# Optimization experiments

Hardware: AMD Instinct MI355X
Metric: run time of the kernel (lower is better)

Reference implementation:

```python
import jax, jax.numpy as jnp
import numpy as np

B, S, D, H = 2, 2048, 512, 8
DK = D // H

def setup_inputs() -> dict:
    key = jax.random.key(0)
    ks = jax.random.split(key, 13)
    inp = {
        'query': jax.random.normal(ks[0], (B, S, D), jnp.float32),
        'key': jax.random.normal(ks[1], (B, S, D), jnp.float32),
        'value': jax.random.normal(ks[2], (B, S, D), jnp.float32),
        'group_prob': jax.random.uniform(ks[3], (B, S, S), jnp.float32),
        'mask': jax.random.randint(ks[4], (B, S, S), 0, 2, jnp.int32),
        'Wq': jax.random.normal(ks[5], (D, D), jnp.float32) * 0.02,
        'bq': jax.random.normal(ks[6], (D,), jnp.float32) * 0.02,
        'Wk': jax.random.normal(ks[7], (D, D), jnp.float32) * 0.02,
        'bk': jax.random.normal(ks[8], (D,), jnp.float32) * 0.02,
        'Wv': jax.random.normal(ks[9], (D, D), jnp.float32) * 0.02,
        'bv': jax.random.normal(ks[10], (D,), jnp.float32) * 0.02,
        'Wo': jax.random.normal(ks[11], (D, D), jnp.float32) * 0.02,
        'bo': jax.random.normal(ks[12], (D,), jnp.float32) * 0.02,
    }
    return inp

def reference(query, key, value, group_prob, mask, Wq, bq, Wk, bk, Wv, bv, Wo, bo):
    # project and split heads: [B,S,D] -> [B,H,S,dk]
    def proj(x, W, b):
        return (x @ W.T + b).reshape(B, S, H, DK).transpose(0, 2, 1, 3)
    q = proj(query, Wq, bq)
    k = proj(key, Wk, bk)
    v = proj(value, Wv, bv)
    scale = 1.0 / np.sqrt(DK).astype(np.float32)
    scores = jnp.einsum('bhqd,bhkd->bhqk', q, k) * scale  # [B,H,S,S]
    # allowed = mask | identity-diagonal; disallowed positions get -1e9
    diag = jnp.eye(S, dtype=bool)
    allowed = (mask.astype(bool) | diag)[:, None, :, :]  # [B,1,S,S]
    scores = jnp.where(allowed, scores, jnp.float32(-1e9))
    p_attn = jax.nn.softmax(scores, axis=-1) * group_prob[:, None, :, :]
    # dropout is identity in eval/deterministic mode
    x = jnp.einsum('bhqk,bhkd->bhqd', p_attn, v)  # [B,H,S,dk]
    x = x.transpose(0, 2, 1, 3).reshape(B, S, D)
    return x @ Wo.T + bo
```

## Files before the change

### kernel.cpp

```cpp
#include <hip/hip_runtime.h>
#include <hip/hip_bf16.h>
#include <cstdint>
#include <cstddef>

typedef __attribute__((ext_vector_type(8))) short bf16x8;
typedef __attribute__((ext_vector_type(4))) float f32x4;
typedef __attribute__((address_space(3))) void lds_void;
typedef const __attribute__((address_space(1))) void g_void;

constexpr int Bc = 2, Sc = 2048, Dc = 512, Hc = 8, DKc = 64;
constexpr int SPLIT = 2;
constexpr int NKT = Sc / 64;
constexpr int KT_PER = NKT / SPLIT;
constexpr float CSC = 0.18033688011112042f;

struct alignas(16) us8 { unsigned short u[8]; };
struct alignas(8) us4 { unsigned short u[4]; };

__device__ __forceinline__ unsigned short f2bf(float x) {
  union { float f; unsigned int u; } v; v.f = x;
  unsigned int r = (v.u + 0x7FFFu + ((v.u >> 16) & 1u)) >> 16;
  return (unsigned short)r;
}

__device__ __forceinline__ us8 cvt8(float4 a, float4 b) {
  us8 o;
  o.u[0] = f2bf(a.x); o.u[1] = f2bf(a.y); o.u[2] = f2bf(a.z); o.u[3] = f2bf(a.w);
  o.u[4] = f2bf(b.x); o.u[5] = f2bf(b.y); o.u[6] = f2bf(b.z); o.u[7] = f2bf(b.w);
  return o;
}

struct CArgs { const float* src[7]; unsigned short* dst[7]; int n8[7]; };

__global__ __launch_bounds__(256)
void cvt_multi(CArgs a)
{
  const int y = blockIdx.y;
  const float* s = a.src[y];
  unsigned short* d = a.dst[y];
  const int n8 = a.n8[y];
  int i = blockIdx.x * blockDim.x + threadIdx.x;
  const int stride = gridDim.x * blockDim.x;
  for (; i < n8; i += stride) {
    float4 va = ((const float4*)s)[(size_t)i * 2];
    float4 vb = ((const float4*)s)[(size_t)i * 2 + 1];
    ((us8*)d)[i] = cvt8(va, vb);
  }
}

__global__ __launch_bounds__(256)
void cvt_mask(const int* __restrict__ m, unsigned long long* __restrict__ out, int ngroups)
{
  const int lane = threadIdx.x & 63;
  int gid = (blockIdx.x * blockDim.x + threadIdx.x) >> 6;
  const int stride = (gridDim.x * blockDim.x) >> 6;
  for (; gid < ngroups; gid += stride) {
    const size_t base = (size_t)gid * 64;
    const int rem = (int)(base & ((size_t)Sc * Sc - 1));
    const int srow = rem >> 11;
    const int k = (rem & (Sc - 1)) + lane;
    const bool pred = (m[base + lane] != 0) || (k == srow);
    unsigned long long bal = __ballot(pred);
    if (lane == 0) out[gid] = bal;
  }
}

struct GArgs {
  const unsigned short* A[3];
  const unsigned short* W[3];
  const float* bias[3];
  void* C[3];
  int mode[3];
};

__global__ __launch_bounds__(256)
void gemm128(GArgs ga)
{
  __shared__ unsigned short As[128][64];
  __shared__ unsigned short Bs[128][64];

  constexpr int K = 512, N = 512;
  const int z = blockIdx.z;
  const unsigned short* Ap = ga.A[z];
  const unsigned short* Wp = ga.W[z];
  const float* bias = ga.bias[z];
  const int mode = ga.mode[z];

  const int tid = threadIdx.x, lane = tid & 63, w = tid >> 6;
  const int m0 = blockIdx.x * 128, n0 = blockIdx.y * 128;
  const int wm = w >> 1, wn = w & 1;
  const int colb = lane & 15, hi = lane >> 4, rowb = hi * 4;
  const int swz = (colb & 7) << 4;

  f32x4 acc[4][4];
#pragma unroll
  for (int i = 0; i < 4; ++i)
#pragma unroll
    for (int j = 0; j < 4; ++j) acc[i][j] = (f32x4){0.f, 0.f, 0.f, 0.f};

  const int lrow8 = lane >> 3;
  const int cb = ((lane & 7) * 16) ^ (lrow8 << 4);

  for (int k0 = 0; k0 < K; k0 += 64) {
    if (k0) __syncthreads();
#pragma unroll
    for (int i = 0; i < 4; ++i) {
      const int obase = w * 1024 + i * 4096;
      const int row = w * 8 + i * 32 + lrow8;
      const unsigned short* asrc = Ap + (size_t)(m0 + row) * K + k0 + (cb >> 1);
      const unsigned short* bsrc = Wp + (size_t)(n0 + row) * K + k0 + (cb >> 1);
      __builtin_amdgcn_global_load_lds((g_void*)asrc, (lds_void*)((char*)&As[0][0] + obase), 16, 0, 0);
      __builtin_amdgcn_global_load_lds((g_void*)bsrc, (lds_void*)((char*)&Bs[0][0] + obase), 16, 0, 0);
    }
    asm volatile("s_waitcnt vmcnt(0)" ::: "memory");
    __syncthreads();

    char* ab = (char*)&As[0][0];
    char* bb = (char*)&Bs[0][0];
#pragma unroll
    for (int kk = 0; kk < 2; ++kk) {
      bf16x8 af[4], bfr[4];
#pragma unroll
      for (int mf = 0; mf < 4; ++mf) {
        const int ar = wm * 64 + mf * 16 + colb;
        af[mf] = *(const bf16x8*)(ab + ar * 128 + ((kk * 64 + hi * 16) ^ swz));
      }
#pragma unroll
      for (int nf = 0; nf < 4; ++nf) {
        const int br = wn * 64 + nf * 16 + colb;
        bfr[nf] = *(const bf16x8*)(bb + br * 128 + ((kk * 64 + hi * 16) ^ swz));
      }
#pragma unroll
      for (int mf = 0; mf < 4; ++mf)
#pragma unroll
        for (int nf = 0; nf < 4; ++nf)
          acc[mf][nf] = __builtin_amdgcn_mfma_f32_16x16x32_bf16(af[mf], bfr[nf], acc[mf][nf], 0, 0, 0);
    }
  }

#pragma unroll
  for (int nf = 0; nf < 4; ++nf) {
    const int gn = n0 + wn * 64 + nf * 16 + colb;
    const float bv = bias[gn];
    if (mode == 1) {
      unsigned short* Cp = (unsigned short*)ga.C[z];
#pragma unroll
      for (int mf = 0; mf < 4; ++mf) {
        const int gm = m0 + wm * 64 + mf * 16 + rowb;
        const int bb_ = gm >> 11, ss = gm & (Sc - 1);
        us4 vv;
#pragma unroll
        for (int rr = 0; rr < 4; ++rr) vv.u[rr] = f2bf(acc[mf][nf][rr] + bv);
        *(us4*)(Cp + ((size_t)bb_ * N + gn) * Sc + ss) = vv;
      }
    } else if (mode == 0) {
      unsigned short* Cp = (unsigned short*)ga.C[z];
#pragma unroll
      for (int mf = 0; mf < 4; ++mf)
#pragma unroll
        for (int rr = 0; rr < 4; ++rr) {
          const int gm = m0 + wm * 64 + mf * 16 + rowb + rr;
          Cp[(size_t)gm * N + gn] = f2bf(acc[mf][nf][rr] + bv);
        }
    } else {
      float* Cp = (float*)ga.C[z];
#pragma unroll
      for (int mf = 0; mf < 4; ++mf)
#pragma unroll
        for (int rr = 0; rr < 4; ++rr) {
          const int gm = m0 + wm * 64 + mf * 16 + rowb + rr;
          Cp[(size_t)gm * N + gn] = acc[mf][nf][rr] + bv;
        }
    }
  }
}

__global__ __launch_bounds__(256, 4)
void attn_split(const unsigned short* __restrict__ Qb,
                const unsigned short* __restrict__ Kb,
                const unsigned short* __restrict__ Vt,
                const float* __restrict__ Gf,
                const unsigned long long* __restrict__ Mb,
                float* __restrict__ Pacc,
                float* __restrict__ Pml)
{
  __shared__ unsigned short Ks[2][64][64];
  __shared__ unsigned short Vs[2][64][64];
  __shared__ unsigned short Ps[4][16][64];

  const int tid = threadIdx.x, lane = tid & 63, wid = tid >> 6;
  const int bh = blockIdx.x, b = bh >> 3, h = bh & 7;
  const int qt = blockIdx.y, q0 = qt * 64;
  const int sp = blockIdx.z;
  const int kt0 = sp * KT_PER;

  const int colb = lane & 15;
  const int hi = lane >> 4;
  const int rowb = hi * 4;
  const int c3s = (colb & 7) << 4;

  bf16x8 qf[2];
  {
    const unsigned short* qp = Qb + ((size_t)(b * Sc + q0 + wid * 16 + colb) * Dc + h * DKc + hi * 8);
    qf[0] = *(const bf16x8*)qp;
    qf[1] = *(const bf16x8*)(qp + 32);
  }

  f32x4 acc[4] = {{0,0,0,0},{0,0,0,0},{0,0,0,0},{0,0,0,0}};
  float mrun = -1e30f, lrun = 0.f;

  auto stageKV = [&](int bufI, int kt) {
    const int k0 = kt * 64;
#pragma unroll
    for (int i = 0; i < 2; ++i) {
      const int obase = wid * 1024 + i * 4096;
      const int row = (obase >> 7) + (lane >> 3);
      const int cb = ((lane & 7) * 16) ^ ((row & 7) << 4);
      const unsigned short* ksrc = Kb + (size_t)(b * Sc + k0 + row) * Dc + h * DKc + (cb >> 1);
      const unsigned short* vsrc = Vt + ((size_t)b * Dc + h * DKc + row) * Sc + k0 + (cb >> 1);
      __builtin_amdgcn_global_load_lds((g_void*)ksrc, (lds_void*)((char*)&Ks[bufI][0][0] + obase), 16, 0, 0);
      __builtin_amdgcn_global_load_lds((g_void*)vsrc, (lds_void*)((char*)&Vs[bufI][0][0] + obase), 16, 0, 0);
    }
  };

  const unsigned long long* mrow = Mb + ((size_t)(b * Sc) + q0 + wid * 16 + colb) * NKT;
  const float* grow = Gf + ((size_t)(b * Sc) + q0 + wid * 16 + colb) * Sc + hi * 4;

  f32x4 gcur[4];
  unsigned long long mcur;
  auto loadGM = [&](int kt, f32x4* gv, unsigned long long& mm) {
    const float* gp = grow + kt * 64;
#pragma unroll
    for (int n = 0; n < 4; ++n) gv[n] = *(const f32x4*)(gp + n * 16);
    mm = mrow[kt];
  };

  stageKV(0, kt0);
  loadGM(kt0, gcur, mcur);
  asm volatile("s_waitcnt vmcnt(0)" ::: "memory");
  __syncthreads();

  int buf = 0;
  char* psbase = (char*)&Ps[wid][0][0];

  for (int j = 0; j < KT_PER; ++j) {
    const int kt = kt0 + j;
    f32x4 gnx[4]; unsigned long long mn_;
    if (j + 1 < KT_PER) {
      stageKV(buf ^ 1, kt + 1);
      loadGM(kt + 1, gnx, mn_);
    }

    f32x4 sf[4] = {{0,0,0,0},{0,0,0,0},{0,0,0,0},{0,0,0,0}};
    char* ksb = (char*)&Ks[buf][0][0];
#pragma unroll
    for (int kk = 0; kk < 2; ++kk) {
#pragma unroll
      for (int n = 0; n < 4; ++n) {
        const int krow = n * 16 + colb;
        bf16x8 kf = *(const bf16x8*)(ksb + krow * 128 + ((kk * 64 + hi * 16) ^ ((krow & 7) << 4)));
        sf[n] = __builtin_amdgcn_mfma_f32_16x16x32_bf16(kf, qf[kk], sf[n], 0, 0, 0);
      }
    }

    const unsigned long long msh = mcur >> (hi * 4);
#pragma unroll
    for (int n = 0; n < 4; ++n) {
#pragma unroll
      for (int rr = 0; rr < 4; ++rr) {
        const bool allowed = ((unsigned int)(msh >> (n * 16 + rr)) & 1u) != 0u;
        sf[n][rr] = allowed ? sf[n][rr] * CSC : -1e30f;
      }
    }

    float tm = sf[0][0];
#pragma unroll
    for (int n = 0; n < 4; ++n)
#pragma unroll
      for (int rr = 0; rr < 4; ++rr) tm = fmaxf(tm, sf[n][rr]);
    tm = fmaxf(tm, __shfl_xor(tm, 16));
    tm = fmaxf(tm, __shfl_xor(tm, 32));

    if (__any(tm > mrun + 8.f)) {
      const float mnew = fmaxf(mrun, tm);
      const float alpha = __builtin_amdgcn_exp2f(mrun - mnew);
      mrun = mnew;
#pragma unroll
      for (int n = 0; n < 4; ++n)
#pragma unroll
        for (int rr = 0; rr < 4; ++rr) acc[n][rr] *= alpha;
      lrun *= alpha;
    }

    float rsum = 0.f;
    unsigned int pw[8];
#pragma unroll
    for (int n = 0; n < 4; ++n) {
#pragma unroll
      for (int s2 = 0; s2 < 2; ++s2) {
        const float p0 = __builtin_amdgcn_exp2f(sf[n][s2 * 2]     - mrun);
        const float p1 = __builtin_amdgcn_exp2f(sf[n][s2 * 2 + 1] - mrun);
        rsum += p0 + p1;
        const float q0v = p0 * gcur[n][s2 * 2], q1v = p1 * gcur[n][s2 * 2 + 1];
        asm("v_cvt_pk_bf16_f32 %0, %1, %2" : "=v"(pw[n * 2 + s2]) : "v"(q0v), "v"(q1v));
      }
    }
    rsum += __shfl_xor(rsum, 16);
    rsum += __shfl_xor(rsum, 32);
    lrun += rsum;

#pragma unroll
    for (int n = 0; n < 4; ++n) {
      const unsigned long long w64 = ((unsigned long long)pw[n * 2 + 1] << 32) | pw[n * 2];
      *(unsigned long long*)(psbase + colb * 128 + ((n * 32 + hi * 8) ^ c3s)) = w64;
    }

    char* vsb = (char*)&Vs[buf][0][0];
#pragma unroll
    for (int kk = 0; kk < 2; ++kk) {
      bf16x8 pf = *(const bf16x8*)(psbase + colb * 128 + ((kk * 64 + hi * 16) ^ c3s));
#pragma unroll
      for (int n = 0; n < 4; ++n) {
        const int vrow = n * 16 + colb;
        bf16x8 vf = *(const bf16x8*)(vsb + vrow * 128 + ((kk * 64 + hi * 16) ^ ((vrow & 7) << 4)));
        acc[n] = __builtin_amdgcn_mfma_f32_16x16x32_bf16(vf, pf, acc[n], 0, 0, 0);
      }
    }

    asm volatile("s_waitcnt vmcnt(0)" ::: "memory");
    __syncthreads();
    buf ^= 1;
    if (j + 1 < KT_PER) {
#pragma unroll
      for (int n = 0; n < 4; ++n) gcur[n] = gnx[n];
      mcur = mn_;
    }
  }

  const size_t blin = ((size_t)bh * 32 + qt) * SPLIT + sp;
  float* pa = Pacc + blin * 4096;
#pragma unroll
  for (int n = 0; n < 4; ++n)
#pragma unroll
    for (int rr = 0; rr < 4; ++rr)
      pa[(size_t)(n * 16 + rowb + rr) * 64 + wid * 16 + colb] = acc[n][rr];
  if (hi == 0) {
    float* pm = Pml + blin * 128;
    pm[wid * 16 + colb] = mrun;
    pm[64 + wid * 16 + colb] = lrun;
  }
}

__global__ __launch_bounds__(256)
void attn_reduce(const float* __restrict__ Pacc, const float* __restrict__ Pml,
                 unsigned short* __restrict__ Xb)
{
  const int gidx = blockIdx.x;
  const int bh = gidx >> 5, qt = gidx & 31;
  const int b = bh >> 3, h = bh & 7;
  const int tid = threadIdx.x;
  const int qi = tid & 63;
  const int d0 = (tid >> 6) * 16;
  const size_t pb = (size_t)gidx * SPLIT;

  float m[SPLIT], l[SPLIT];
  float mstar = -3.0e38f;
#pragma unroll
  for (int s = 0; s < SPLIT; ++s) {
    m[s] = Pml[(pb + s) * 128 + qi];
    l[s] = Pml[(pb + s) * 128 + 64 + qi];
    mstar = fmaxf(mstar, m[s]);
  }
  float w[SPLIT], denom = 0.f;
#pragma unroll
  for (int s = 0; s < SPLIT; ++s) { w[s] = __builtin_amdgcn_exp2f(m[s] - mstar); denom += w[s] * l[s]; }
  const float inv = 1.0f / denom;

  unsigned short vals[16];
#pragma unroll
  for (int j = 0; j < 16; ++j) {
    float a = 0.f;
#pragma unroll
    for (int s = 0; s < SPLIT; ++s)
      a += w[s] * Pacc[(pb + s) * 4096 + (size_t)(d0 + j) * 64 + qi];
    vals[j] = f2bf(a * inv);
  }
  unsigned short* xp = Xb + ((size_t)(b * Sc) + qt * 64 + qi) * Dc + h * DKc + d0;
  *(us8*)xp = *(us8*)&vals[0];
  *(us8*)(xp + 8) = *(us8*)&vals[8];
}

extern "C" void kernel_launch(void* const* d_in, const int* in_sizes, int n_in,
                              void* d_out, int out_size, void* d_ws, size_t ws_size,
                              hipStream_t stream)
{
  const float* query = (const float*)d_in[0];
  const float* key_  = (const float*)d_in[1];
  const float* value = (const float*)d_in[2];
  const float* gprob = (const float*)d_in[3];
  const int*   mask  = (const int*)d_in[4];
  const float* Wq = (const float*)d_in[5];
  const float* bq = (const float*)d_in[6];
  const float* Wk = (const float*)d_in[7];
  const float* bk = (const float*)d_in[8];
  const float* Wv = (const float*)d_in[9];
  const float* bv = (const float*)d_in[10];
  const float* Wo = (const float*)d_in[11];
  const float* bo = (const float*)d_in[12];
  float* out = (float*)d_out;

  const size_t elems = (size_t)Bc * Sc * Dc;
  const size_t gelems = (size_t)Bc * Sc * Sc;
  const size_t welems = (size_t)Dc * Dc;

  char* base = (char*)d_ws;
  unsigned short* Qb = (unsigned short*)(base);
  unsigned short* Kb = Qb + elems;
  unsigned short* Vt = Kb + elems;
  unsigned short* Xb = Vt + elems;
  unsigned long long* Mbits = (unsigned long long*)(Xb + elems);
  char* shared_region = (char*)(Mbits + gelems / 64);
  unsigned short* Ain = (unsigned short*)shared_region;
  unsigned short* Bin = Ain + elems;
  unsigned short* Cin = Bin + elems;
  float* Pacc = (float*)shared_region;
  float* Pml  = Pacc + (size_t)(Bc * Hc) * 32 * SPLIT * 4096;
  unsigned short* Wqb = (unsigned short*)(shared_region + (18u << 20));
  unsigned short* Wkb = Wqb + welems;
  unsigned short* Wvb = Wkb + welems;
  unsigned short* Wob = Wvb + welems;

  CArgs ca;
  ca.src[0] = query; ca.dst[0] = Ain; ca.n8[0] = (int)(elems / 8);
  ca.src[1] = key_;  ca.dst[1] = Bin; ca.n8[1] = (int)(elems / 8);
  ca.src[2] = value; ca.dst[2] = Cin; ca.n8[2] = (int)(elems / 8);
  ca.src[3] = Wq;    ca.dst[3] = Wqb; ca.n8[3] = (int)(welems / 8);
  ca.src[4] = Wk;    ca.dst[4] = Wkb; ca.n8[4] = (int)(welems / 8);
  ca.src[5] = Wv;    ca.dst[5] = Wvb; ca.n8[5] = (int)(welems / 8);
  ca.src[6] = Wo;    ca.dst[6] = Wob; ca.n8[6] = (int)(welems / 8);
  hipLaunchKernelGGL(cvt_multi, dim3(128, 7), dim3(256), 0, stream, ca);
  hipLaunchKernelGGL(cvt_mask, dim3(2048), dim3(256), 0, stream, mask, Mbits, (int)(gelems / 64));

  GArgs gq;
  gq.A[0] = Ain; gq.W[0] = Wqb; gq.bias[0] = bq; gq.C[0] = (void*)Qb; gq.mode[0] = 0;
  gq.A[1] = Bin; gq.W[1] = Wkb; gq.bias[1] = bk; gq.C[1] = (void*)Kb; gq.mode[1] = 0;
  gq.A[2] = Cin; gq.W[2] = Wvb; gq.bias[2] = bv; gq.C[2] = (void*)Vt; gq.mode[2] = 1;
  hipLaunchKernelGGL(gemm128, dim3(32, 4, 3), dim3(256), 0, stream, gq);

  dim3 ga(Bc * Hc, Sc / 64, SPLIT);
  hipLaunchKernelGGL(attn_split, ga, dim3(256), 0, stream, Qb, Kb, Vt, gprob, Mbits, Pacc, Pml);
  hipLaunchKernelGGL(attn_reduce, dim3(Bc * Hc * 32), dim3(256), 0, stream, Pacc, Pml, Xb);

  GArgs go;
  go.A[0] = Xb; go.W[0] = Wob; go.bias[0] = bo; go.C[0] = (void*)out; go.mode[0] = 2;
  go.A[1] = Xb; go.W[1] = Wob; go.bias[1] = bo; go.C[1] = (void*)out; go.mode[1] = 2;
  go.A[2] = Xb; go.W[2] = Wob; go.bias[2] = bo; go.C[2] = (void*)out; go.mode[2] = 2;
  hipLaunchKernelGGL(gemm128, dim3(32, 4, 1), dim3(256), 0, stream, go);
}
```

Measured before the change: 110.7 us.

## Prefuse mask into bf16 group_prob, fold softmax scale into Q, add MFMA priority

The mask-packing pass now also turns group_prob into bf16, zeroing disallowed positions, and still writes the packed mask bits. The attention kernel therefore reads half as many bytes of group_prob per head, and it drops the per-score mask select and scale multiply. The softmax scale is folded into the Q projection epilogue. The mask bits now only gate the row-sum accumulation. s_setprio hints are placed around the MFMA blocks in both the GEMM and attention kernels. In exchange the pre-pass reads the full fp32 group_prob and writes an extra 16MB buffer. The running max is also taken over unmasked scores, which changes the numerics slightly.

```diff
diff --git a/kernel.cpp b/kernel.cpp
--- a/kernel.cpp
+++ b/kernel.cpp
@@ -21,6 +21,11 @@
   union { float f; unsigned int u; } v; v.f = x;
   unsigned int r = (v.u + 0x7FFFu + ((v.u >> 16) & 1u)) >> 16;
   return (unsigned short)r;
+}
+
+__device__ __forceinline__ float bf2f(unsigned short u) {
+  union { unsigned int u; float f; } v; v.u = ((unsigned int)u) << 16;
+  return v.f;
 }
 
 __device__ __forceinline__ us8 cvt8(float4 a, float4 b) {
@@ -49,19 +54,37 @@
 }
 
 __global__ __launch_bounds__(256)
-void cvt_mask(const int* __restrict__ m, unsigned long long* __restrict__ out, int ngroups)
+void cvt_gmask(const float* __restrict__ g, const int* __restrict__ m,
+               unsigned short* __restrict__ ge, unsigned long long* __restrict__ mb,
+               int ngr8)
 {
   const int lane = threadIdx.x & 63;
-  int gid = (blockIdx.x * blockDim.x + threadIdx.x) >> 6;
-  const int stride = (gridDim.x * blockDim.x) >> 6;
-  for (; gid < ngroups; gid += stride) {
-    const size_t base = (size_t)gid * 64;
+  int i = blockIdx.x * blockDim.x + threadIdx.x;
+  const int stride = gridDim.x * blockDim.x;
+  for (; i < ngr8; i += stride) {
+    const size_t base = (size_t)i * 8;
     const int rem = (int)(base & ((size_t)Sc * Sc - 1));
-    const int srow = rem >> 11;
-    const int k = (rem & (Sc - 1)) + lane;
-    const bool pred = (m[base + lane] != 0) || (k == srow);
-    unsigned long long bal = __ballot(pred);
-    if (lane == 0) out[gid] = bal;
+    const int row = rem >> 11;
+    const int col0 = rem & (Sc - 1);
+    int4 m0 = *(const int4*)(m + base);
+    int4 m1 = *(const int4*)(m + base + 4);
+    float4 g0 = *(const float4*)(g + base);
+    float4 g1 = *(const float4*)(g + base + 4);
+    const int mm[8] = {m0.x, m0.y, m0.z, m0.w, m1.x, m1.y, m1.z, m1.w};
+    const float gg[8] = {g0.x, g0.y, g0.z, g0.w, g1.x, g1.y, g1.z, g1.w};
+    us8 o; unsigned int pm = 0;
+#pragma unroll
+    for (int j = 0; j < 8; ++j) {
+      const bool pred = (mm[j] != 0) || (col0 + j == row);
+      o.u[j] = pred ? f2bf(gg[j]) : (unsigned short)0;
+      pm |= (pred ? 1u : 0u) << j;
+    }
+    ((us8*)ge)[i] = o;
+    unsigned long long v = (unsigned long long)pm << ((lane & 7) * 8);
+    v |= __shfl_xor(v, 1);
+    v |= __shfl_xor(v, 2);
+    v |= __shfl_xor(v, 4);
+    if ((lane & 7) == 0) mb[i >> 3] = v;
   }
 }
 
@@ -71,6 +94,7 @@
   const float* bias[3];
   void* C[3];
   int mode[3];
+  float osc[3];
 };
 
 __global__ __launch_bounds__(256)
@@ -85,6 +109,7 @@
   const unsigned short* Wp = ga.W[z];
   const float* bias = ga.bias[z];
   const int mode = ga.mode[z];
+  const float osc = ga.osc[z];
 
   const int tid = threadIdx.x, lane = tid & 63, w = tid >> 6;
   const int m0 = blockIdx.x * 128, n0 = blockIdx.y * 128;
@@ -130,11 +155,13 @@
         const int br = wn * 64 + nf * 16 + colb;
         bfr[nf] = *(const bf16x8*)(bb + br * 128 + ((kk * 64 + hi * 16) ^ swz));
       }
+      __builtin_amdgcn_s_setprio(1);
 #pragma unroll
       for (int mf = 0; mf < 4; ++mf)
 #pragma unroll
         for (int nf = 0; nf < 4; ++nf)
           acc[mf][nf] = __builtin_amdgcn_mfma_f32_16x16x32_bf16(af[mf], bfr[nf], acc[mf][nf], 0, 0, 0);
+      __builtin_amdgcn_s_setprio(0);
     }
   }
 
@@ -160,7 +187,7 @@
 #pragma unroll
         for (int rr = 0; rr < 4; ++rr) {
           const int gm = m0 + wm * 64 + mf * 16 + rowb + rr;
-          Cp[(size_t)gm * N + gn] = f2bf(acc[mf][nf][rr] + bv);
+          Cp[(size_t)gm * N + gn] = f2bf((acc[mf][nf][rr] + bv) * osc);
         }
     } else {
       float* Cp = (float*)ga.C[z];
@@ -179,7 +206,7 @@
 void attn_split(const unsigned short* __restrict__ Qb,
                 const unsigned short* __restrict__ Kb,
                 const unsigned short* __restrict__ Vt,
-                const float* __restrict__ Gf,
+                const unsigned short* __restrict__ Gb,
                 const unsigned long long* __restrict__ Mb,
                 float* __restrict__ Pacc,
                 float* __restrict__ Pml)
@@ -224,14 +251,14 @@
   };
 
   const unsigned long long* mrow = Mb + ((size_t)(b * Sc) + q0 + wid * 16 + colb) * NKT;
-  const float* grow = Gf + ((size_t)(b * Sc) + q0 + wid * 16 + colb) * Sc + hi * 4;
-
-  f32x4 gcur[4];
+  const unsigned short* growb = Gb + ((size_t)(b * Sc) + q0 + wid * 16 + colb) * Sc + hi * 4;
+
+  us4 gcur[4];
   unsigned long long mcur;
-  auto loadGM = [&](int kt, f32x4* gv, unsigned long long& mm) {
-    const float* gp = grow + kt * 64;
-#pragma unroll
-    for (int n = 0; n < 4; ++n) gv[n] = *(const f32x4*)(gp + n * 16);
+  auto loadGM = [&](int kt, us4* gv, unsigned long long& mm) {
+    const unsigned short* gp = growb + kt * 64;
+#pragma unroll
+    for (int n = 0; n < 4; ++n) gv[n] = *(const us4*)(gp + n * 16);
     mm = mrow[kt];
   };
 
@@ -245,7 +272,7 @@
 
   for (int j = 0; j < KT_PER; ++j) {
     const int kt = kt0 + j;
-    f32x4 gnx[4]; unsigned long long mn_;
+    us4 gnx[4]; unsigned long long mn_;
     if (j + 1 < KT_PER) {
       stageKV(buf ^ 1, kt + 1);
       loadGM(kt + 1, gnx, mn_);
@@ -253,6 +280,7 @@
 
     f32x4 sf[4] = {{0,0,0,0},{0,0,0,0},{0,0,0,0},{0,0,0,0}};
     char* ksb = (char*)&Ks[buf][0][0];
+    __builtin_amdgcn_s_setprio(1);
 #pragma unroll
     for (int kk = 0; kk < 2; ++kk) {
 #pragma unroll
@@ -262,16 +290,7 @@
         sf[n] = __builtin_amdgcn_mfma_f32_16x16x32_bf16(kf, qf[kk], sf[n], 0, 0, 0);
       }
     }
-
-    const unsigned long long msh = mcur >> (hi * 4);
-#pragma unroll
-    for (int n = 0; n < 4; ++n) {
-#pragma unroll
-      for (int rr = 0; rr < 4; ++rr) {
-        const bool allowed = ((unsigned int)(msh >> (n * 16 + rr)) & 1u) != 0u;
-        sf[n][rr] = allowed ? sf[n][rr] * CSC : -1e30f;
-      }
-    }
+    __builtin_amdgcn_s_setprio(0);
 
     float tm = sf[0][0];
 #pragma unroll
@@ -292,16 +311,22 @@
       lrun *= alpha;
     }
 
+    const unsigned long long msh = mcur >> (hi * 4);
+    const unsigned int mlo = (unsigned int)msh, mhi2 = (unsigned int)(msh >> 32);
     float rsum = 0.f;
     unsigned int pw[8];
 #pragma unroll
     for (int n = 0; n < 4; ++n) {
 #pragma unroll
       for (int s2 = 0; s2 < 2; ++s2) {
-        const float p0 = __builtin_amdgcn_exp2f(sf[n][s2 * 2]     - mrun);
-        const float p1 = __builtin_amdgcn_exp2f(sf[n][s2 * 2 + 1] - mrun);
-        rsum += p0 + p1;
-        const float q0v = p0 * gcur[n][s2 * 2], q1v = p1 * gcur[n][s2 * 2 + 1];
+        const int i0 = s2 * 2, i1 = s2 * 2 + 1;
+        const float p0 = __builtin_amdgcn_exp2f(sf[n][i0] - mrun);
+        const float p1 = __builtin_amdgcn_exp2f(sf[n][i1] - mrun);
+        const float b0 = (float)((n < 2 ? (mlo >> (n * 16 + i0)) : (mhi2 >> ((n - 2) * 16 + i0))) & 1u);
+        const float b1 = (float)((n < 2 ? (mlo >> (n * 16 + i1)) : (mhi2 >> ((n - 2) * 16 + i1))) & 1u);
+        rsum = fmaf(p0, b0, rsum);
+        rsum = fmaf(p1, b1, rsum);
+        const float q0v = p0 * bf2f(gcur[n].u[i0]), q1v = p1 * bf2f(gcur[n].u[i1]);
         asm("v_cvt_pk_bf16_f32 %0, %1, %2" : "=v"(pw[n * 2 + s2]) : "v"(q0v), "v"(q1v));
       }
     }
@@ -316,6 +341,7 @@
     }
 
     char* vsb = (char*)&Vs[buf][0][0];
+    __builtin_amdgcn_s_setprio(1);
 #pragma unroll
     for (int kk = 0; kk < 2; ++kk) {
       bf16x8 pf = *(const bf16x8*)(psbase + colb * 128 + ((kk * 64 + hi * 16) ^ c3s));
@@ -326,6 +352,7 @@
         acc[n] = __builtin_amdgcn_mfma_f32_16x16x32_bf16(vf, pf, acc[n], 0, 0, 0);
       }
     }
+    __builtin_amdgcn_s_setprio(0);
 
     asm volatile("s_waitcnt vmcnt(0)" ::: "memory");
     __syncthreads();
@@ -418,7 +445,8 @@
   unsigned short* Kb = Qb + elems;
   unsigned short* Vt = Kb + elems;
   unsigned short* Xb = Vt + elems;
-  unsigned long long* Mbits = (unsigned long long*)(Xb + elems);
+  unsigned short* Gb = Xb + elems;
+  unsigned long long* Mbits = (unsigned long long*)(Gb + gelems);
   char* shared_region = (char*)(Mbits + gelems / 64);
   unsigned short* Ain = (unsigned short*)shared_region;
   unsigned short* Bin = Ain + elems;
@@ -439,21 +467,21 @@
   ca.src[5] = Wv;    ca.dst[5] = Wvb; ca.n8[5] = (int)(welems / 8);
   ca.src[6] = Wo;    ca.dst[6] = Wob; ca.n8[6] = (int)(welems / 8);
   hipLaunchKernelGGL(cvt_multi, dim3(128, 7), dim3(256), 0, stream, ca);
-  hipLaunchKernelGGL(cvt_mask, dim3(2048), dim3(256), 0, stream, mask, Mbits, (int)(gelems / 64));
+  hipLaunchKernelGGL(cvt_gmask, dim3(2048), dim3(256), 0, stream, gprob, mask, Gb, Mbits, (int)(gelems / 8));
 
   GArgs gq;
-  gq.A[0] = Ain; gq.W[0] = Wqb; gq.bias[0] = bq; gq.C[0] = (void*)Qb; gq.mode[0] = 0;
-  gq.A[1] = Bin; gq.W[1] = Wkb; gq.bias[1] = bk; gq.C[1] = (void*)Kb; gq.mode[1] = 0;
-  gq.A[2] = Cin; gq.W[2] = Wvb; gq.bias[2] = bv; gq.C[2] = (void*)Vt; gq.mode[2] = 1;
+  gq.A[0] = Ain; gq.W[0] = Wqb; gq.bias[0] = bq; gq.C[0] = (void*)Qb; gq.mode[0] = 0; gq.osc[0] = CSC;
+  gq.A[1] = Bin; gq.W[1] = Wkb; gq.bias[1] = bk; gq.C[1] = (void*)Kb; gq.mode[1] = 0; gq.osc[1] = 1.0f;
+  gq.A[2] = Cin; gq.W[2] = Wvb; gq.bias[2] = bv; gq.C[2] = (void*)Vt; gq.mode[2] = 1; gq.osc[2] = 1.0f;
   hipLaunchKernelGGL(gemm128, dim3(32, 4, 3), dim3(256), 0, stream, gq);
 
   dim3 ga(Bc * Hc, Sc / 64, SPLIT);
-  hipLaunchKernelGGL(attn_split, ga, dim3(256), 0, stream, Qb, Kb, Vt, gprob, Mbits, Pacc, Pml);
+  hipLaunchKernelGGL(attn_split, ga, dim3(256), 0, stream, Qb, Kb, Vt, Gb, Mbits, Pacc, Pml);
   hipLaunchKernelGGL(attn_reduce, dim3(Bc * Hc * 32), dim3(256), 0, stream, Pacc, Pml, Xb);
 
   GArgs go;
-  go.A[0] = Xb; go.W[0] = Wob; go.bias[0] = bo; go.C[0] = (void*)out; go.mode[0] = 2;
-  go.A[1] = Xb; go.W[1] = Wob; go.bias[1] = bo; go.C[1] = (void*)out; go.mode[1] = 2;
-  go.A[2] = Xb; go.W[2] = Wob; go.bias[2] = bo; go.C[2] = (void*)out; go.mode[2] = 2;
+  go.A[0] = Xb; go.W[0] = Wob; go.bias[0] = bo; go.C[0] = (void*)out; go.mode[0] = 2; go.osc[0] = 1.0f;
+  go.A[1] = Xb; go.W[1] = Wob; go.bias[1] = bo; go.C[1] = (void*)out; go.mode[1] = 2; go.osc[1] = 1.0f;
+  go.A[2] = Xb; go.W[2] = Wob; go.bias[2] = bo; go.C[2] = (void*)out; go.mode[2] = 2; go.osc[2] = 1.0f;
   hipLaunchKernelGGL(gemm128, dim3(32, 4, 1), dim3(256), 0, stream, go);
 }
```

Measured after the change: 116.6 us. +5.3%, slower.
